# Kernel tuning notes

Measured on AMD Instinct MI355X. Metric: run time of the kernel, lower is better.

## Reference

```python
import jax, jax.numpy as jnp
import numpy as np

N_HEAD, D_HEAD = 16, 64
D_MODEL = N_HEAD * D_HEAD
QLEN, MLEN, BSZ = 1024, 1024, 4
KLEN = QLEN + MLEN
LN_EPS = 1e-5


def setup_inputs() -> dict:
    key = jax.random.key(0)
    ks = jax.random.split(key, 8)
    w = jax.random.normal(ks[0], (QLEN, BSZ, D_MODEL), jnp.float32)
    r = jax.random.normal(ks[1], (KLEN, D_MODEL), jnp.float32)
    mems = jax.random.normal(ks[2], (MLEN, BSZ, D_MODEL), jnp.float32)
    # causal mask over (qlen, klen): query i may attend keys j <= i + MLEN
    i = jnp.arange(QLEN)[:, None]
    j = jnp.arange(KLEN)[None, :]
    attn_mask = j > (i + MLEN)  # True = masked
    s = 1.0 / np.sqrt(D_MODEL)
    qkv_w = jax.random.normal(ks[3], (3 * D_MODEL, D_MODEL), jnp.float32) * s
    r_net_w = jax.random.normal(ks[4], (D_MODEL, D_MODEL), jnp.float32) * s
    o_w = jax.random.normal(ks[5], (D_MODEL, D_MODEL), jnp.float32) * s
    r_r_bias = jax.random.normal(ks[6], (N_HEAD, D_HEAD), jnp.float32) * 0.02
    r_w_bias = jax.random.normal(ks[7], (N_HEAD, D_HEAD), jnp.float32) * 0.02
    ln_gamma = jnp.ones((D_MODEL,), jnp.float32)
    ln_beta = jnp.zeros((D_MODEL,), jnp.float32)
    return {"w": w, "r": r, "mems": mems, "attn_mask": attn_mask,
            "qkv_w": qkv_w, "r_net_w": r_net_w, "o_w": o_w,
            "r_r_bias": r_r_bias, "r_w_bias": r_w_bias,
            "ln_gamma": ln_gamma, "ln_beta": ln_beta}


def _layer_norm(x, g, b):
    mu = jnp.mean(x, axis=-1, keepdims=True)
    var = jnp.var(x, axis=-1, keepdims=True)
    return (x - mu) * jax.lax.rsqrt(var + LN_EPS) * g + b


def _rel_shift(x):
    # x: [qlen, rlen, bsz, n_head]
    q, rl, b, n = x.shape
    x_pad = jnp.pad(x, ((0, 0), (1, 0), (0, 0), (0, 0)))  # zero row at front of axis 1
    x_pad = x_pad.reshape(rl + 1, q, b, n)
    return x_pad[1:].reshape(q, rl, b, n)


def reference(w, r, mems, attn_mask, qkv_w, r_net_w, o_w, r_r_bias, r_w_bias, ln_gamma, ln_beta):
    qlen, bsz = w.shape[0], w.shape[1]
    cat = jnp.concatenate([mems, w], axis=0)  # [klen, b, d]
    klen = cat.shape[0]
    w_heads = cat @ qkv_w.T  # [klen, b, 3*d]
    r_head_k = (r @ r_net_w.T).reshape(r.shape[0], N_HEAD, D_HEAD)  # [rlen, n, dh]
    w_q, w_k, w_v = jnp.split(w_heads, 3, axis=-1)
    w_q = w_q[-qlen:].reshape(qlen, bsz, N_HEAD, D_HEAD)
    w_k = w_k.reshape(klen, bsz, N_HEAD, D_HEAD)
    w_v = w_v.reshape(klen, bsz, N_HEAD, D_HEAD)

    scale = 1.0 / np.sqrt(D_HEAD)
    AC = jnp.einsum('ibnd,jbnd->ijbn', w_q + r_w_bias, w_k)
    BD = _rel_shift(jnp.einsum('ibnd,jnd->ijbn', w_q + r_r_bias, r_head_k))
    attn_score = (AC + BD) * scale
    attn_score = jnp.where(attn_mask[None, :, :, None].transpose(1, 2, 0, 3), -1e30, attn_score) if False else \
        jnp.where(attn_mask[:, :, None, None], jnp.float32(-1e30), attn_score)
    attn_prob = jax.nn.softmax(attn_score, axis=1)
    attn_vec = jnp.einsum('ijbn,jbnd->ibnd', attn_prob, w_v)
    attn_vec = attn_vec.reshape(qlen, bsz, N_HEAD * D_HEAD)
    attn_out = attn_vec @ o_w.T
    return _layer_norm(w + attn_out, ln_gamma, ln_beta)
```

## Files before the change

### kernel.cpp

```cpp
#include <hip/hip_runtime.h>
#include <hip/hip_bf16.h>

typedef __attribute__((ext_vector_type(8))) short short8;
typedef __attribute__((ext_vector_type(4))) float f32x4;
typedef __hip_bfloat16 bf16;

#define NHEAD 16
#define DHEAD 64
#define DMODEL 1024
#define QLEN 1024
#define MLEN 1024
#define BSZ 4
#define KLEN 2048
#define LOG2E 1.44269504088896f

__device__ __forceinline__ float fast_exp2(float x) {
#if __has_builtin(__builtin_amdgcn_exp2f)
  return __builtin_amdgcn_exp2f(x);
#else
  return exp2f(x);
#endif
}

__device__ __forceinline__ short8 ld8(const bf16* p) { return *(const short8*)p; }
__device__ __forceinline__ void st8(bf16* p, short8 v) { *(short8*)p = v; }
__device__ __forceinline__ f32x4 mfma16(short8 a, short8 b, f32x4 c) {
  return __builtin_amdgcn_mfma_f32_16x16x32_bf16(a, b, c, 0, 0, 0);
}
__device__ __forceinline__ float bfu2f(unsigned short u) {
  unsigned int x = ((unsigned int)u) << 16;
  return __uint_as_float(x);
}
__device__ __forceinline__ unsigned short f2bfu(float f) {
  bf16 t = __float2bfloat16(f);
  return *(unsigned short*)&t;
}
__device__ __forceinline__ unsigned short f2bfu_fast(float f) {
  return (unsigned short)((__float_as_uint(f) + 0x8000u) >> 16);
}
__device__ __forceinline__ bf16 bf16_raw(unsigned short u) {
  bf16 t; *(unsigned short*)&t = u; return t;
}
__device__ __forceinline__ void async16(const bf16* g, bf16* l) {
  __builtin_amdgcn_global_load_lds(
      (const __attribute__((address_space(1))) unsigned int*)g,
      (__attribute__((address_space(3))) unsigned int*)l, 16, 0, 0);
}

__device__ __forceinline__ int probe_is_f32(const unsigned short* wq) {
  const int lane = threadIdx.x & 63;
  unsigned short u = wq[2 * lane];
  int e = (u >> 7) & 0xFF;
  unsigned long long m = __ballot(e >= 100 && e <= 134);
  return __popcll(m) < 32;
}

#define DPPF(x, ctrl, rm) \
  __int_as_float(__builtin_amdgcn_update_dpp( \
      __float_as_int(x), __float_as_int(x), (ctrl), (rm), 0xF, false))

__global__ __launch_bounds__(256) void convert_inputs(
    const void* s0, const void* s1, const void* s2,
    const void* s3, const void* s4, const void* s5,
    bf16* d0, bf16* d1, bf16* d2, bf16* d3, bf16* d4, bf16* d5)
{
  const int isf = probe_is_f32((const unsigned short*)s0);
  const int b = blockIdx.x;
  const void* src; bf16* dst; int lb;
  if (b < 2048)      { src = s0; dst = d0; lb = b; }
  else if (b < 4096) { src = s1; dst = d1; lb = b - 2048; }
  else if (b < 5120) { src = s2; dst = d2; lb = b - 4096; }
  else if (b < 6656) { src = s3; dst = d3; lb = b - 5120; }
  else if (b < 7168) { src = s4; dst = d4; lb = b - 6656; }
  else               { src = s5; dst = d5; lb = b - 7168; }
  const size_t idx = ((size_t)lb * 256 + threadIdx.x) * 8;
  if (isf) {
    const f32x4* f = (const f32x4*)src;
    f32x4 a = f[idx >> 2];
    f32x4 c = f[(idx >> 2) + 1];
    short8 v;
    v[0] = (short)f2bfu(a[0]); v[1] = (short)f2bfu(a[1]);
    v[2] = (short)f2bfu(a[2]); v[3] = (short)f2bfu(a[3]);
    v[4] = (short)f2bfu(c[0]); v[5] = (short)f2bfu(c[1]);
    v[6] = (short)f2bfu(c[2]); v[7] = (short)f2bfu(c[3]);
    st8(dst + idx, v);
  } else {
    st8(dst + idx, ld8((const bf16*)src + idx));
  }
}

__device__ __forceinline__ void gemm_core64(
    const bf16* const ap[4], const bf16* const bp[4],
    bf16* As, bf16* Bs, int wv, int wm, int wn, int lr, int lg,
    f32x4 acc[4][4])
{
  const int sx = lr & 7;
  for (int k0 = 0; k0 < DMODEL; k0 += 64) {
    #pragma unroll
    for (int p = 0; p < 4; ++p) {
      async16(ap[p] + k0, As + (wv * 32 + p * 8) * 64);
      async16(bp[p] + k0, Bs + (wv * 32 + p * 8) * 64);
    }
    __syncthreads();
    #pragma unroll
    for (int ks = 0; ks < 2; ++ks) {
      const int col = (((ks * 4 + lg) ^ sx) << 3);
      short8 bfr[4];
      #pragma unroll
      for (int nt = 0; nt < 4; ++nt) bfr[nt] = ld8(Bs + (wn * 64 + nt * 16 + lr) * 64 + col);
      #pragma unroll
      for (int mt = 0; mt < 4; ++mt) {
        short8 af = ld8(As + (wm * 64 + mt * 16 + lr) * 64 + col);
        #pragma unroll
        for (int nt = 0; nt < 4; ++nt)
          acc[mt][nt] = mfma16(af, bfr[nt], acc[mt][nt]);
      }
    }
    __syncthreads();
  }
}

__global__ __launch_bounds__(256) void qkv_gemm(
    const bf16* __restrict__ w, const bf16* __restrict__ mems,
    const bf16* __restrict__ qkv_w,
    const bf16* __restrict__ r, const bf16* __restrict__ rnet_w,
    const void* __restrict__ r_w_bias, const void* __restrict__ r_r_bias,
    const void* __restrict__ worig,
    bf16* __restrict__ qac, bf16* __restrict__ qbd,
    bf16* __restrict__ kbuf, bf16* __restrict__ vbuf,
    bf16* __restrict__ rkbuf)
{
  const int id = blockIdx.x;
  int sec, bx, by;
  if (id < 256)       { sec = 0; bx = id >> 5;                    by = 32 + (id & 31); }
  else if (id < 768)  { sec = 1; int t = id - 256;  bx = 8  + (t >> 6); by = t & 63; }
  else if (id < 1280) { sec = 2; int t = id - 768;  bx = 16 + (t >> 6); by = t & 63; }
  else                { sec = 3; int t = id - 1280; bx = 24 + (t >> 4); by = t & 15; }
  __shared__ bf16 sh[16384];
  bf16* As = sh;
  bf16* Bs = sh + 8192;
  const int tid = threadIdx.x;
  const int lane = tid & 63, wv = tid >> 6;
  const int wm = wv >> 1, wn = wv & 1;
  const int lr = lane & 15, lg = lane >> 4;
  const int lr8 = lane >> 3;
  const int ucol = ((lane & 7) ^ lr8) * 8;
  const bf16 *ap[4], *bp[4];
  #pragma unroll
  for (int p = 0; p < 4; ++p) {
    int arow = wv * 32 + p * 8 + lr8;
    if (sec == 3) {
      ap[p] = r + (size_t)(by * 128 + arow) * DMODEL + ucol;
      bp[p] = rnet_w + (size_t)((bx - 24) * 128 + arow) * DMODEL + ucol;
    } else {
      int m = by * 128 + arow;
      int j = m >> 2, b = m & 3;
      ap[p] = ((j < MLEN) ? (mems + ((size_t)(j * BSZ + b)) * DMODEL)
                          : (w + ((size_t)((j - MLEN) * BSZ + b)) * DMODEL)) + ucol;
      bp[p] = qkv_w + (size_t)(bx * 128 + arow) * DMODEL + ucol;
    }
  }
  f32x4 zero = {0.f, 0.f, 0.f, 0.f};
  f32x4 acc[4][4];
  #pragma unroll
  for (int a = 0; a < 4; ++a)
    #pragma unroll
    for (int c2 = 0; c2 < 4; ++c2) acc[a][c2] = zero;
  gemm_core64(ap, bp, As, Bs, wv, wm, wn, lr, lg, acc);

  if (sec == 2) {
    #pragma unroll
    for (int nt = 0; nt < 4; ++nt) {
      int n = wn * 64 + nt * 16 + lr;
      #pragma unroll
      for (int mt = 0; mt < 4; ++mt) {
        int jl = wm * 16 + mt * 4 + lg;
        #pragma unroll
        for (int rr = 0; rr < 4; ++rr) {
          int x = rr * 32 + jl;
          sh[n * 128 + (((x >> 4) ^ (n & 7)) << 4) + (x & 15)] =
              __float2bfloat16(acc[mt][nt][rr]);
        }
      }
    }
    __syncthreads();
    const int grp = lane >> 3, sl = lane & 7;
    const int hbase = (bx - 16) * 2;
    #pragma unroll
    for (int i = 0; i < 16; ++i) {
      int idx = i * 32 + wv * 8 + grp;
      int n = idx >> 2, bb = idx & 3;
      int x0 = bb * 32 + sl * 4;
      ushort4 v4 = *(const ushort4*)(sh + n * 128 + (((x0 >> 4) ^ (n & 7)) << 4) + (x0 & 15));
      int hh = hbase + (n >> 6), dd = n & 63;
      *(ushort4*)(vbuf + ((size_t)(bb * NHEAD + hh) * DHEAD + dd) * KLEN + by * 32 + sl * 4) = v4;
    }
    return;
  }
  if (sec == 3) {
    #pragma unroll
    for (int nt = 0; nt < 4; ++nt) {
      int col = (bx - 24) * 128 + wn * 64 + nt * 16 + lr;
      int h = col >> 6, d = col & 63;
      #pragma unroll
      for (int mt = 0; mt < 4; ++mt) {
        #pragma unroll
        for (int rr = 0; rr < 4; ++rr) {
          int m = by * 128 + wm * 64 + mt * 16 + lg * 4 + rr;
          rkbuf[((size_t)h * KLEN + m) * DHEAD + d] = __float2bfloat16(acc[mt][nt][rr]);
        }
      }
    }
    return;
  }
  int isf = 0;
  if (sec == 0) isf = probe_is_f32((const unsigned short*)worig);
  const float QSC = 0.125f * LOG2E;
  #pragma unroll
  for (int nt = 0; nt < 4; ++nt) {
    int col = bx * 128 + wn * 64 + nt * 16 + lr;
    int nn = col & 1023;
    int h = nn >> 6, d = nn & 63;
    float rwb = 0.f, rrb = 0.f;
    if (sec == 0) {
      if (isf) { rwb = ((const float*)r_w_bias)[nn]; rrb = ((const float*)r_r_bias)[nn]; }
      else { rwb = __bfloat162float(((const bf16*)r_w_bias)[nn]);
             rrb = __bfloat162float(((const bf16*)r_r_bias)[nn]); }
    }
    #pragma unroll
    for (int mt = 0; mt < 4; ++mt) {
      #pragma unroll
      for (int rr = 0; rr < 4; ++rr) {
        int m = by * 128 + wm * 64 + mt * 16 + lg * 4 + rr;
        int j = m >> 2, b = m & 3;
        float v = acc[mt][nt][rr];
        if (sec == 0) {
          int i = j - MLEN;
          size_t base = (((size_t)(b * NHEAD + h)) * QLEN + i) * DHEAD + d;
          qac[base] = __float2bfloat16((v + rwb) * QSC);
          qbd[base] = __float2bfloat16((v + rrb) * QSC);
        } else {
          kbuf[(((size_t)(b * NHEAD + h)) * KLEN + j) * DHEAD + d] = __float2bfloat16(v);
        }
      }
    }
  }
}

#define GROT(Gx) \
    _Pragma("unroll") for (int ct = 0; ct < 5; ++ct) \
      _Pragma("unroll") for (int rr = 0; rr < 4; ++rr) { \
        float y = Gx[ct][rr]; \
        y = DPPF(y, 0x124, 0xA);            \
        y = DPPF(y, 0x128, 0xC);            \
        Gx[ct][rr] = y; \
      }

#define RRBODY(RR, CTRL, Sx, Gx, lsx, pwx, igb) { \
    const int di = g * 4 + RR; \
    float sh[5]; \
    _Pragma("unroll") for (int ct = 0; ct < 5; ++ct) { \
      float y = Gx[ct][RR]; \
      sh[ct] = __int_as_float(__builtin_amdgcn_update_dpp( \
          __float_as_int(y), __float_as_int(y), (CTRL), 0xF, 0xF, false)); \
    } \
    float sv[4]; \
    _Pragma("unroll") for (int jt = 0; jt < 4; ++jt) { \
      float bd = (c > di) ? sh[jt + 1] : sh[jt]; \
      sv[jt] = Sx[jt][RR] + bd; \
    } \
    if (maskt) { \
      const int ig = (igb) + di; \
      _Pragma("unroll") for (int jt = 0; jt < 4; ++jt) \
        if (j0 + jt * 16 + c > ig + MLEN) sv[jt] = -1e30f; \
    } \
    _Pragma("unroll") for (int jt = 0; jt < 4; ++jt) { \
      float pv = fast_exp2(sv[jt]); \
      lsx[RR] += pv; \
      pwx[di * 64 + ((((jt * 2) + (c >> 3)) ^ (di & 7)) << 3) + (c & 7)] = \
          bf16_raw(f2bfu_fast(pv)); \
    } \
  }

__global__ __launch_bounds__(256, 2) void attn_kernel(
    const bf16* __restrict__ qac, const bf16* __restrict__ qbd,
    const bf16* __restrict__ kbuf, const bf16* __restrict__ vbuf,
    const bf16* __restrict__ rkbuf, bf16* __restrict__ av)
{
  const int id = blockIdx.x;
  const int idh = id >> 6;
  const int qt = (id < 256) ? (7 - idh) : (idh - 4);
  const int bh = id & 63;
  const int b = bh >> 4, h = bh & 15;
  const int i0 = qt * 128;
  __shared__ bf16 Ks[64 * 64];
  __shared__ bf16 Vt[2 * 64 * 64];
  __shared__ bf16 Rs[192 * 64];
  __shared__ bf16 Ps[8 * 16 * 64];
  const int tid = threadIdx.x;
  const int wv = tid >> 6, lane = tid & 63;
  const int c = lane & 15, g = lane >> 4;
  const size_t bhb = (size_t)(b * NHEAD + h);
  const int lr8 = lane >> 3;
  const int ucol = ((lane & 7) ^ lr8) * 8;
  const int sw0 = ((0 + g) ^ (c & 7)) * 8;
  const int sw1 = ((4 + g) ^ (c & 7)) * 8;

  short8 qaf0[2], qaf1[2], qbf0[2], qbf1[2];
  {
    const size_t qr0 = (bhb * QLEN + i0 + wv * 32 + c) * DHEAD;
    const size_t qr1 = qr0 + 16 * DHEAD;
    #pragma unroll
    for (int ks = 0; ks < 2; ++ks) {
      qaf0[ks] = ld8(qac + qr0 + ks * 32 + g * 8);
      qbf0[ks] = ld8(qbd + qr0 + ks * 32 + g * 8);
      qaf1[ks] = ld8(qac + qr1 + ks * 32 + g * 8);
      qbf1[ks] = ld8(qbd + qr1 + ks * 32 + g * 8);
    }
  }
  f32x4 zero = {0.f, 0.f, 0.f, 0.f};
  f32x4 O0[4], O1[4];
  #pragma unroll
  for (int dt = 0; dt < 4; ++dt) { O0[dt] = zero; O1[dt] = zero; }
  float ls0[4] = {0.f, 0.f, 0.f, 0.f};
  float ls1[4] = {0.f, 0.f, 0.f, 0.f};

  bf16* pw0 = Ps + (wv * 2 + 0) * 1024;
  bf16* pw1 = Ps + (wv * 2 + 1) * 1024;
  const bf16* kc = Ks + c * 64;

  const int ofs0 = 112 - wv * 32;
  const int ofs1 = ofs0 - 16;
  const int igb0 = i0 + wv * 32;
  const int igb1 = igb0 + 16;

  const int ntiles = 2 * qt + 18;
  const int wlo0 = 896 - i0;
  const bf16* rkh = rkbuf + (size_t)h * KLEN * DHEAD;

  #pragma unroll
  for (int p = 0; p < 2; ++p) {
    int r0 = wv * 16 + p * 8;
    async16(kbuf + (bhb * KLEN + r0 + lr8) * DHEAD + ucol, Ks + r0 * 64);
  }
  #pragma unroll
  for (int p = 0; p < 6; ++p) {
    int r0 = wv * 48 + p * 8;
    async16(rkh + (size_t)(wlo0 + r0 + lr8) * DHEAD + ucol, Rs + r0 * 64);
  }
  #pragma unroll
  for (int p = 0; p < 2; ++p) {
    int r0 = wv * 16 + p * 8;
    async16(vbuf + (bhb * DHEAD + r0 + lr8) * KLEN + ucol, Vt + r0 * 64);
  }

  const bf16 *rb0 = Rs, *rb1 = Rs + 4096, *rb2 = Rs + 8192;

  for (int t = 0; t < ntiles; ++t) {
    const int j0 = t * 64;
    const bool maskt = (t >= ntiles - 2);
    asm volatile("s_waitcnt vmcnt(0)" ::: "memory");
    __builtin_amdgcn_s_barrier();
    __builtin_amdgcn_sched_barrier(0);
    const bf16* vb = Vt + (t & 1) * 4096 + c * 64;

    f32x4 S0[4], S1[4];
    #pragma unroll
    for (int jt = 0; jt < 4; ++jt) { S0[jt] = zero; S1[jt] = zero; }
    #pragma unroll
    for (int ks = 0; ks < 2; ++ks) {
      const int sw = ks ? sw1 : sw0;
      #pragma unroll
      for (int jt = 0; jt < 4; ++jt) {
        short8 kf = ld8(kc + jt * 1024 + sw);
        S0[jt] = mfma16(qaf0[ks], kf, S0[jt]);
        S1[jt] = mfma16(qaf1[ks], kf, S1[jt]);
      }
    }
    f32x4 G0[5];
    #pragma unroll
    for (int ct = 0; ct < 5; ++ct) G0[ct] = zero;
    #pragma unroll
    for (int ks = 0; ks < 2; ++ks) {
      const int sw = ks ? sw1 : sw0;
      #pragma unroll
      for (int ct = 0; ct < 5; ++ct) {
        int rel = ofs0 + 16 * ct;
        int qq = rel >> 6;
        const bf16* rp = (qq == 0) ? rb0 : ((qq == 1) ? rb1 : rb2);
        G0[ct] = mfma16(qbf0[ks], ld8(rp + (c + (rel & 63)) * 64 + sw), G0[ct]);
      }
    }
    GROT(G0)
    RRBODY(0, 0x121, S0, G0, ls0, pw0, igb0)
    RRBODY(1, 0x122, S0, G0, ls0, pw0, igb0)
    RRBODY(2, 0x123, S0, G0, ls0, pw0, igb0)
    RRBODY(3, 0x124, S0, G0, ls0, pw0, igb0)
    f32x4 G1[5];
    #pragma unroll
    for (int ct = 0; ct < 5; ++ct) G1[ct] = zero;
    #pragma unroll
    for (int ks = 0; ks < 2; ++ks) {
      const int sw = ks ? sw1 : sw0;
      #pragma unroll
      for (int ct = 0; ct < 5; ++ct) {
        int rel = ofs1 + 16 * ct;
        int qq = rel >> 6;
        const bf16* rp = (qq == 0) ? rb0 : ((qq == 1) ? rb1 : rb2);
        G1[ct] = mfma16(qbf1[ks], ld8(rp + (c + (rel & 63)) * 64 + sw), G1[ct]);
      }
    }
    asm volatile("s_waitcnt lgkmcnt(0)" ::: "memory");
    __builtin_amdgcn_s_barrier();
    __builtin_amdgcn_sched_barrier(0);
    if (t + 1 < ntiles) {
      const int j1 = j0 + 64;
      const int snew = wlo0 + 192 + j0;
      bf16* vstg = Vt + ((t + 1) & 1) * 4096;
      #pragma unroll
      for (int p = 0; p < 2; ++p) {
        int r0 = wv * 16 + p * 8;
        async16(kbuf + (bhb * KLEN + j1 + r0 + lr8) * DHEAD + ucol, Ks + r0 * 64);
        async16(rkh + (size_t)(snew + r0 + lr8) * DHEAD + ucol,
                (bf16*)rb0 + r0 * 64);
        async16(vbuf + (bhb * DHEAD + r0 + lr8) * KLEN + j1 + ucol,
                vstg + r0 * 64);
      }
      __builtin_amdgcn_sched_barrier(0);
    }
    GROT(G1)
    RRBODY(0, 0x121, S1, G1, ls1, pw1, igb1)
    RRBODY(1, 0x122, S1, G1, ls1, pw1, igb1)
    RRBODY(2, 0x123, S1, G1, ls1, pw1, igb1)
    RRBODY(3, 0x124, S1, G1, ls1, pw1, igb1)
    #pragma unroll
    for (int ks = 0; ks < 2; ++ks) {
      const int psw = (((ks * 4 + g) ^ (c & 7)) << 3);
      short8 pf0 = ld8(pw0 + c * 64 + psw);
      short8 pf1 = ld8(pw1 + c * 64 + psw);
      const int sw = ks ? sw1 : sw0;
      #pragma unroll
      for (int dt = 0; dt < 4; ++dt) {
        short8 vf = ld8(vb + dt * 1024 + sw);
        O0[dt] = mfma16(pf0, vf, O0[dt]);
        O1[dt] = mfma16(pf1, vf, O1[dt]);
      }
    }
    const bf16* tb = rb0; rb0 = rb1; rb1 = rb2; rb2 = tb;
  }
  #pragma unroll
  for (int rr = 0; rr < 4; ++rr) {
    float s = ls0[rr];
    s += DPPF(s, 0xB1, 0xF);
    s += DPPF(s, 0x4E, 0xF);
    s += DPPF(s, 0x141, 0xF);
    s += DPPF(s, 0x140, 0xF);
    ls0[rr] = s;
    float s1 = ls1[rr];
    s1 += DPPF(s1, 0xB1, 0xF);
    s1 += DPPF(s1, 0x4E, 0xF);
    s1 += DPPF(s1, 0x141, 0xF);
    s1 += DPPF(s1, 0x140, 0xF);
    ls1[rr] = s1;
  }
  #pragma unroll
  for (int rr = 0; rr < 4; ++rr) {
    float inv0 = 1.0f / ls0[rr];
    float inv1 = 1.0f / ls1[rr];
    #pragma unroll
    for (int dt = 0; dt < 4; ++dt) {
      int d = dt * 16 + c;
      int ig0 = igb0 + g * 4 + rr;
      int ig1 = igb1 + g * 4 + rr;
      av[((size_t)ig0 * BSZ + b) * DMODEL + h * DHEAD + d] =
          __float2bfloat16(O0[dt][rr] * inv0);
      av[((size_t)ig1 * BSZ + b) * DMODEL + h * DHEAD + d] =
          __float2bfloat16(O1[dt][rr] * inv1);
    }
  }
}

__global__ __launch_bounds__(256) void out_gemm(
    const bf16* __restrict__ av, const bf16* __restrict__ o_w,
    bf16* __restrict__ ao)
{
  const int id = blockIdx.x;
  const int bx = id >> 5, by = id & 31;
  __shared__ bf16 As[128 * 64];
  __shared__ bf16 Bs[128 * 64];
  const int tid = threadIdx.x;
  const int lane = tid & 63, wv = tid >> 6;
  const int wm = wv >> 1, wn = wv & 1;
  const int lr = lane & 15, lg = lane >> 4;
  const int lr8 = lane >> 3;
  const int ucol = ((lane & 7) ^ lr8) * 8;
  const bf16 *ap[4], *bp[4];
  #pragma unroll
  for (int p = 0; p < 4; ++p) {
    int arow = wv * 32 + p * 8 + lr8;
    ap[p] = av + (size_t)(by * 128 + arow) * DMODEL + ucol;
    bp[p] = o_w + (size_t)(bx * 128 + arow) * DMODEL + ucol;
  }
  f32x4 zero = {0.f, 0.f, 0.f, 0.f};
  f32x4 acc[4][4];
  #pragma unroll
  for (int a = 0; a < 4; ++a)
    #pragma unroll
    for (int c2 = 0; c2 < 4; ++c2) acc[a][c2] = zero;
  gemm_core64(ap, bp, As, Bs, wv, wm, wn, lr, lg, acc);
  #pragma unroll
  for (int nt = 0; nt < 4; ++nt) {
    int col = bx * 128 + wn * 64 + nt * 16 + lr;
    #pragma unroll
    for (int mt = 0; mt < 4; ++mt) {
      #pragma unroll
      for (int rr = 0; rr < 4; ++rr) {
        int m = by * 128 + wm * 64 + mt * 16 + lg * 4 + rr;
        ao[(size_t)m * DMODEL + col] = __float2bfloat16(acc[mt][nt][rr]);
      }
    }
  }
}

__global__ __launch_bounds__(256) void ln_kernel(
    const void* __restrict__ wz, const bf16* __restrict__ ao,
    const void* __restrict__ gz, const void* __restrict__ bz,
    void* __restrict__ outz)
{
  const int m = blockIdx.x;
  const int tid = threadIdx.x;
  const int isf = probe_is_f32((const unsigned short*)wz);
  ushort4 au = ((const ushort4*)ao)[m * 256 + tid];
  float a4[4];
  a4[0] = bfu2f(au.x); a4[1] = bfu2f(au.y); a4[2] = bfu2f(au.z); a4[3] = bfu2f(au.w);
  float x[4], gg[4], bb[4];
  if (isf) {
    f32x4 w4 = ((const f32x4*)wz)[m * 256 + tid];
    f32x4 g4 = ((const f32x4*)gz)[tid];
    f32x4 b4 = ((const f32x4*)bz)[tid];
    #pragma unroll
    for (int k = 0; k < 4; ++k) { x[k] = w4[k] + a4[k]; gg[k] = g4[k]; bb[k] = b4[k]; }
  } else {
    ushort4 w4 = ((const ushort4*)wz)[m * 256 + tid];
    ushort4 g4 = ((const ushort4*)gz)[tid];
    ushort4 b4 = ((const ushort4*)bz)[tid];
    x[0] = bfu2f(w4.x) + a4[0]; x[1] = bfu2f(w4.y) + a4[1];
    x[2] = bfu2f(w4.z) + a4[2]; x[3] = bfu2f(w4.w) + a4[3];
    gg[0] = bfu2f(g4.x); gg[1] = bfu2f(g4.y); gg[2] = bfu2f(g4.z); gg[3] = bfu2f(g4.w);
    bb[0] = bfu2f(b4.x); bb[1] = bfu2f(b4.y); bb[2] = bfu2f(b4.z); bb[3] = bfu2f(b4.w);
  }
  float s = x[0] + x[1] + x[2] + x[3];
  float s2 = x[0]*x[0] + x[1]*x[1] + x[2]*x[2] + x[3]*x[3];
  #pragma unroll
  for (int o = 32; o > 0; o >>= 1) {
    s += __shfl_xor(s, o, 64);
    s2 += __shfl_xor(s2, o, 64);
  }
  __shared__ float red[8];
  const int wv = tid >> 6, lane = tid & 63;
  if (lane == 0) { red[wv] = s; red[4 + wv] = s2; }
  __syncthreads();
  s = red[0] + red[1] + red[2] + red[3];
  s2 = red[4] + red[5] + red[6] + red[7];
  const float mu = s * (1.0f / DMODEL);
  const float var = s2 * (1.0f / DMODEL) - mu * mu;
  const float rstd = rsqrtf(var + 1e-5f);
  float y[4];
  #pragma unroll
  for (int k = 0; k < 4; ++k) y[k] = (x[k] - mu) * rstd * gg[k] + bb[k];
  if (isf) {
    f32x4 o4; o4[0] = y[0]; o4[1] = y[1]; o4[2] = y[2]; o4[3] = y[3];
    ((f32x4*)outz)[m * 256 + tid] = o4;
  } else {
    ushort4 o4;
    o4.x = f2bfu(y[0]); o4.y = f2bfu(y[1]); o4.z = f2bfu(y[2]); o4.w = f2bfu(y[3]);
    ((ushort4*)outz)[m * 256 + tid] = o4;
  }
}

extern "C" void kernel_launch(void* const* d_in, const int* in_sizes, int n_in,
                              void* d_out, int out_size, void* d_ws, size_t ws_size,
                              hipStream_t stream) {
  (void)in_sizes; (void)n_in; (void)out_size; (void)ws_size;
  const void* w      = d_in[0];
  const void* r      = d_in[1];
  const void* mems   = d_in[2];
  const void* qkv_w  = d_in[4];
  const void* rnet_w = d_in[5];
  const void* o_w    = d_in[6];
  const void* rrb    = d_in[7];
  const void* rwb    = d_in[8];
  const void* ln_g   = d_in[9];
  const void* ln_b   = d_in[10];

  char* ws = (char*)d_ws;
  const size_t MB = 1ull << 20;
  bf16* cw    = (bf16*)(ws + 0 * MB);
  bf16* cmems = (bf16*)(ws + 8 * MB);
  bf16* cr    = (bf16*)(ws + 16 * MB);
  bf16* cqkvw = (bf16*)(ws + 20 * MB);
  bf16* crnet = (bf16*)(ws + 26 * MB);
  bf16* cow   = (bf16*)(ws + 28 * MB);
  bf16* qac   = (bf16*)(ws + 31 * MB);
  bf16* qbd   = (bf16*)(ws + 39 * MB);
  bf16* kbuf  = (bf16*)(ws + 47 * MB);
  bf16* vbuf  = (bf16*)(ws + 63 * MB);
  bf16* rkbuf = (bf16*)(ws + 79 * MB);
  bf16* av    = (bf16*)(ws + 83 * MB);
  bf16* ao    = (bf16*)(ws + 0 * MB);

  convert_inputs<<<7680, 256, 0, stream>>>(w, mems, r, qkv_w, rnet_w, o_w,
                                           cw, cmems, cr, cqkvw, crnet, cow);
  qkv_gemm<<<1408, 256, 0, stream>>>(cw, cmems, cqkvw, cr, crnet,
                                     rwb, rrb, w,
                                     qac, qbd, kbuf, vbuf, rkbuf);
  attn_kernel<<<512, 256, 0, stream>>>(qac, qbd, kbuf, vbuf, rkbuf, av);
  out_gemm<<<256, 256, 0, stream>>>(av, cow, ao);
  ln_kernel<<<dim3(4096), 256, 0, stream>>>(w, ao, ln_g, ln_b, d_out);
}
```

Before: 284.3 us.

## Compute softmax row sums via MFMA with ones vector and add setprio

After: 285.8 us. About the same (+0.5%).

```diff
diff --git a/kernel.cpp b/kernel.cpp
--- a/kernel.cpp
+++ b/kernel.cpp
@@ -256,7 +256,7 @@
         Gx[ct][rr] = y; \
       }
 
-#define RRBODY(RR, CTRL, Sx, Gx, lsx, pwx, igb) { \
+#define RRBODY(RR, CTRL, Sx, Gx, pwx, igb) { \
     const int di = g * 4 + RR; \
     float sh[5]; \
     _Pragma("unroll") for (int ct = 0; ct < 5; ++ct) { \
@@ -276,7 +276,6 @@
     } \
     _Pragma("unroll") for (int jt = 0; jt < 4; ++jt) { \
       float pv = fast_exp2(sv[jt]); \
-      lsx[RR] += pv; \
       pwx[di * 64 + ((((jt * 2) + (c >> 3)) ^ (di & 7)) << 3) + (c & 7)] = \
           bf16_raw(f2bfu_fast(pv)); \
     } \
@@ -318,12 +317,15 @@
       qbf1[ks] = ld8(qbd + qr1 + ks * 32 + g * 8);
     }
   }
+  short8 vones;
+  #pragma unroll
+  for (int j = 0; j < 8; ++j) vones[j] = (short)0x3F80;
+
   f32x4 zero = {0.f, 0.f, 0.f, 0.f};
   f32x4 O0[4], O1[4];
   #pragma unroll
   for (int dt = 0; dt < 4; ++dt) { O0[dt] = zero; O1[dt] = zero; }
-  float ls0[4] = {0.f, 0.f, 0.f, 0.f};
-  float ls1[4] = {0.f, 0.f, 0.f, 0.f};
+  f32x4 OL0 = zero, OL1 = zero;
 
   bf16* pw0 = Ps + (wv * 2 + 0) * 1024;
   bf16* pw1 = Ps + (wv * 2 + 1) * 1024;
@@ -367,6 +369,7 @@
     f32x4 S0[4], S1[4];
     #pragma unroll
     for (int jt = 0; jt < 4; ++jt) { S0[jt] = zero; S1[jt] = zero; }
+    __builtin_amdgcn_s_setprio(1);
     #pragma unroll
     for (int ks = 0; ks < 2; ++ks) {
       const int sw = ks ? sw1 : sw0;
@@ -391,14 +394,16 @@
         G0[ct] = mfma16(qbf0[ks], ld8(rp + (c + (rel & 63)) * 64 + sw), G0[ct]);
       }
     }
+    __builtin_amdgcn_s_setprio(0);
     GROT(G0)
-    RRBODY(0, 0x121, S0, G0, ls0, pw0, igb0)
-    RRBODY(1, 0x122, S0, G0, ls0, pw0, igb0)
-    RRBODY(2, 0x123, S0, G0, ls0, pw0, igb0)
-    RRBODY(3, 0x124, S0, G0, ls0, pw0, igb0)
+    RRBODY(0, 0x121, S0, G0, pw0, igb0)
+    RRBODY(1, 0x122, S0, G0, pw0, igb0)
+    RRBODY(2, 0x123, S0, G0, pw0, igb0)
+    RRBODY(3, 0x124, S0, G0, pw0, igb0)
     f32x4 G1[5];
     #pragma unroll
     for (int ct = 0; ct < 5; ++ct) G1[ct] = zero;
+    __builtin_amdgcn_s_setprio(1);
     #pragma unroll
     for (int ks = 0; ks < 2; ++ks) {
       const int sw = ks ? sw1 : sw0;
@@ -410,6 +415,7 @@
         G1[ct] = mfma16(qbf1[ks], ld8(rp + (c + (rel & 63)) * 64 + sw), G1[ct]);
       }
     }
+    __builtin_amdgcn_s_setprio(0);
     asm volatile("s_waitcnt lgkmcnt(0)" ::: "memory");
     __builtin_amdgcn_s_barrier();
     __builtin_amdgcn_sched_barrier(0);
@@ -429,15 +435,18 @@
       __builtin_amdgcn_sched_barrier(0);
     }
     GROT(G1)
-    RRBODY(0, 0x121, S1, G1, ls1, pw1, igb1)
-    RRBODY(1, 0x122, S1, G1, ls1, pw1, igb1)
-    RRBODY(2, 0x123, S1, G1, ls1, pw1, igb1)
-    RRBODY(3, 0x124, S1, G1, ls1, pw1, igb1)
+    RRBODY(0, 0x121, S1, G1, pw1, igb1)
+    RRBODY(1, 0x122, S1, G1, pw1, igb1)
+    RRBODY(2, 0x123, S1, G1, pw1, igb1)
+    RRBODY(3, 0x124, S1, G1, pw1, igb1)
+    __builtin_amdgcn_s_setprio(1);
     #pragma unroll
     for (int ks = 0; ks < 2; ++ks) {
       const int psw = (((ks * 4 + g) ^ (c & 7)) << 3);
       short8 pf0 = ld8(pw0 + c * 64 + psw);
       short8 pf1 = ld8(pw1 + c * 64 + psw);
+      OL0 = mfma16(pf0, vones, OL0);
+      OL1 = mfma16(pf1, vones, OL1);
       const int sw = ks ? sw1 : sw0;
       #pragma unroll
       for (int dt = 0; dt < 4; ++dt) {
@@ -446,27 +455,13 @@
         O1[dt] = mfma16(pf1, vf, O1[dt]);
       }
     }
+    __builtin_amdgcn_s_setprio(0);
     const bf16* tb = rb0; rb0 = rb1; rb1 = rb2; rb2 = tb;
   }
   #pragma unroll
   for (int rr = 0; rr < 4; ++rr) {
-    float s = ls0[rr];
-    s += DPPF(s, 0xB1, 0xF);
-    s += DPPF(s, 0x4E, 0xF);
-    s += DPPF(s, 0x141, 0xF);
-    s += DPPF(s, 0x140, 0xF);
-    ls0[rr] = s;
-    float s1 = ls1[rr];
-    s1 += DPPF(s1, 0xB1, 0xF);
-    s1 += DPPF(s1, 0x4E, 0xF);
-    s1 += DPPF(s1, 0x141, 0xF);
-    s1 += DPPF(s1, 0x140, 0xF);
-    ls1[rr] = s1;
-  }
-  #pragma unroll
-  for (int rr = 0; rr < 4; ++rr) {
-    float inv0 = 1.0f / ls0[rr];
-    float inv1 = 1.0f / ls1[rr];
+    float inv0 = 1.0f / OL0[rr];
+    float inv1 = 1.0f / OL1[rr];
     #pragma unroll
     for (int dt = 0; dt < 4; ++dt) {
       int d = dt * 16 + c;
```
